# Kernel optimization log

Measured on AMD Instinct MI355X. Metric: run time of the kernel, lower is better.

The kernel has to match this reference:

```python
import jax, jax.numpy as jnp
import numpy as np

B, S, V = 8, 8192, 64
D, DV, DT, H = 256, 32, 256, 8
DH = D // H

def setup_inputs() -> dict:
    key = jax.random.key(0)
    ks = jax.random.split(key, 24)
    def p(i, shape, s=0.02):
        return jax.random.normal(ks[i], shape, jnp.float32) * s
    return {
        'times': jax.random.uniform(ks[0], (B, S), jnp.float32),
        'feature_ids': jax.random.randint(ks[1], (B, S), 0, V),
        'values': jax.random.normal(ks[2], (B, S), jnp.float32),
        'valid_mask': jax.random.randint(ks[3], (B, S), 0, 2).astype(bool),
        'me_w': p(4, (D,), 1.0), 'me_b': p(5, (D,)),
        'var_emb': p(6, (V, DV), 1.0),
        'time_w': p(7, (DT,), 1.0), 'time_b': p(8, (DT,)),
        'agg_w': p(9, (D + DT, D - DV)), 'agg_b': p(10, (D - DV,)),
        'wq': p(11, (D, D)), 'bq': p(12, (D,)),
        'wk': p(13, (D, D)), 'bk': p(14, (D,)),
        'wv': p(15, (D, D)), 'bv': p(16, (D,)),
        'wo': p(17, (D, D)), 'bo': p(18, (D,)),
        'cw1': p(19, (D, D)), 'cb1': p(20, (D,)),
        'cw2': p(21, (D, 1)), 'cb2': p(22, (1,)),
    }

def reference(times, feature_ids, values, valid_mask,
              me_w, me_b, var_emb, time_w, time_b, agg_w, agg_b,
              wq, bq, wk, bk, wv, bv, wo, bo, cw1, cb1, cw2, cb2):
    # Embeddings: measurement [B,S,D], variate [B,S,DV], time [B,S,DT]
    e_l = values[..., None] * me_w + me_b
    v_l = var_emb[feature_ids]
    u_l = times[..., None] * time_w + time_b
    eu = jnp.concatenate([e_l, u_l], axis=-1)                   # [B,S,D+DT]
    h_l = jnp.concatenate([v_l, eu @ agg_w + agg_b], axis=-1)   # [B,S,D]

    # Vectorized masked segment mean per variate (replaces Python loop)
    var_mask = (feature_ids[:, None, :] == jnp.arange(V)[None, :, None]) \
               & valid_mask[:, None, :]                         # [B,V,S] bool
    mf = var_mask.astype(h_l.dtype)
    sums = jnp.einsum('bvs,bsd->bvd', mf, h_l)
    counts = jnp.clip(mf.sum(-1), 1.0)                          # [B,V]
    f_mean = sums / counts[..., None]                           # [B,V,D]

    # Grouped cross-attention: one query per variate, shared K/V = h_l
    kpm = ~var_mask                                             # key padding mask
    all_masked = ~var_mask.any(-1)                              # [B,V]
    kpm = kpm.at[:, :, 0].set(kpm[:, :, 0] & ~all_masked)       # unmask pos 0 if empty

    q = (f_mean @ wq + bq).reshape(B, V, H, DH)
    k = (h_l @ wk + bk).reshape(B, S, H, DH)
    v = (h_l @ wv + bv).reshape(B, S, H, DH)
    scores = jnp.einsum('bvhd,bshd->bvhs', q, k) / np.sqrt(DH)  # [B,V,H,S]
    neg = jnp.finfo(scores.dtype).min
    scores = jnp.where(kpm[:, :, None, :], neg, scores)
    attn = jax.nn.softmax(scores, axis=-1)
    ctx = jnp.einsum('bvhs,bshd->bvhd', attn, v).reshape(B, V, D)
    f_var = ctx @ wo + bo                                       # [B,V,D]

    f = f_var.mean(axis=1)                                      # [B,D]
    out = jax.nn.relu(f @ cw1 + cb1) @ cw2 + cb2                # [B,1]
    return out
```

## Files before the change

### kernel.cpp

```cpp
#include <hip/hip_runtime.h>
#include <hip/hip_bf16.h>
#include <math.h>

#define BB 8
#define SS 8192
#define VV 64
#define AGG_OUT 224

#define WS_FLAGS 0
#define WS_A     16
#define WS_C     240
#define WS_D     464
#define WS_AQ    688
#define WS_CQ    944
#define WS_DQ    1200
#define WS_AK    1456
#define WS_CK    1712
#define WS_DK    1968
#define WS_AV    2224
#define WS_CV    2480
#define WS_DV    2736
#define WS_WQE   2992
#define WS_WKE   19376
#define WS_WVE   35760
#define WS_CSUM  52144
#define WS_BINS  54192
#define WS_COEF  66480
#define WS_SP    82864

__device__ __forceinline__ float ldf(const void* p, int idx, int fm) {
  if (fm) {
    unsigned int u = ((const unsigned short*)p)[idx];
    return __uint_as_float(u << 16);
  }
  return ((const float*)p)[idx];
}

__device__ __forceinline__ bool mask_at(const void* p, int idx, int mm) {
  switch (mm) {
    case 0: return ((const int*)p)[idx] != 0;
    case 1: return ((const float*)p)[idx] != 0.0f;
    case 2: return ((const unsigned short*)p)[idx] != 0;
    default: return ((const unsigned char*)p)[idx] != 0;
  }
}

__device__ __forceinline__ unsigned int fkey(float f) {
  unsigned int u = __float_as_uint(f);
  return (u & 0x80000000u) ? ~u : (u | 0x80000000u);
}
__device__ __forceinline__ float funkey(unsigned int k) {
  unsigned int u = (k & 0x80000000u) ? (k ^ 0x80000000u) : ~k;
  return __uint_as_float(u);
}

__device__ __forceinline__ int detect_fm_block(const void* times) {
  __shared__ int cntR;
  int tid = threadIdx.x;
  if (tid == 0) cntR = 0;
  __syncthreads();
  const unsigned int* tw = (const unsigned int*)times;
  int local = 0;
  for (int i = tid; i < 1024; i += 256) {
    unsigned int lo = tw[i] & 0xFFFFu;
    if (lo >= 0x3800u && lo < 0x3F80u) local++;
  }
  atomicAdd(&cntR, local);
  __syncthreads();
  int r = (cntR > 512) ? 1 : 0;
  __syncthreads();
  return r;
}

__device__ __forceinline__ int detect_mm_block(const void* mask) {
  __shared__ int f01, ff32, fbf;
  int tid = threadIdx.x;
  if (tid == 0) { f01 = 1; ff32 = 1; fbf = 1; }
  __syncthreads();
  const unsigned int* mw = (const unsigned int*)mask;
  int l01 = 1, lf32 = 1, lbf = 1;
  for (int i = tid; i < 2048; i += 256) {
    unsigned int w = mw[i];
    if (w > 1u) l01 = 0;
    if (!(w == 0u || w == 0x3F800000u)) lf32 = 0;
    unsigned int h0 = w & 0xFFFFu, h1 = w >> 16;
    if (!((h0 == 0u || h0 == 0x3F80u) && (h1 == 0u || h1 == 0x3F80u))) lbf = 0;
  }
  if (!l01) atomicAnd(&f01, 0);
  if (!lf32) atomicAnd(&ff32, 0);
  if (!lbf) atomicAnd(&fbf, 0);
  __syncthreads();
  int r = f01 ? 0 : (ff32 ? 1 : (fbf ? 2 : 3));
  __syncthreads();
  return r;
}

__global__ void __launch_bounds__(256) k_front(const void* times, const void* values,
                                               const int* fids, const void* mask,
                                               const void* me_w, const void* me_b,
                                               const void* time_w, const void* time_b,
                                               const void* agg_w, const void* agg_b,
                                               float* ws) {
  int blk = blockIdx.x, tid = threadIdx.x;
  if (blk < 224) {
    int fm = detect_fm_block(times);
    int j = blk, i = tid;
    float w0 = ldf(agg_w, i * AGG_OUT + j, fm);
    float w1 = ldf(agg_w, (256 + i) * AGG_OUT + j, fm);
    float sa = ldf(me_w, i, fm) * w0;
    float sc = ldf(time_w, i, fm) * w1;
    float sd = ldf(me_b, i, fm) * w0 + ldf(time_b, i, fm) * w1;
    #pragma unroll
    for (int off = 32; off >= 1; off >>= 1) {
      sa += __shfl_xor(sa, off);
      sc += __shfl_xor(sc, off);
      sd += __shfl_xor(sd, off);
    }
    __shared__ float r[3][4];
    int wid = i >> 6;
    if ((i & 63) == 0) { r[0][wid] = sa; r[1][wid] = sc; r[2][wid] = sd; }
    __syncthreads();
    if (i == 0) {
      ws[WS_A + j] = r[0][0] + r[0][1] + r[0][2] + r[0][3];
      ws[WS_C + j] = r[1][0] + r[1][1] + r[1][2] + r[1][3];
      ws[WS_D + j] = r[2][0] + r[2][1] + r[2][2] + r[2][3] + ldf(agg_b, j, fm);
    }
  } else if (blk < 288) {
    int fm = detect_fm_block(times);
    int mm = detect_mm_block(mask);
    int sblk = blk - 224, b = sblk >> 3, chunk = sblk & 7;
    __shared__ float hc[64], hsv[64], hst[64];
    __shared__ unsigned int hvn[64], hvx[64], htn[64], htx[64];
    if (tid < 64) {
      hc[tid] = 0.f; hsv[tid] = 0.f; hst[tid] = 0.f;
      hvn[tid] = 0xFFFFFFFFu; hvx[tid] = 0u;
      htn[tid] = 0xFFFFFFFFu; htx[tid] = 0u;
    }
    __syncthreads();
    #pragma unroll
    for (int k = 0; k < 4; k++) {
      int idx = b * SS + chunk * 1024 + k * 256 + tid;
      if (mask_at(mask, idx, mm)) {
        int f = fids[idx];
        float val = ldf(values, idx, fm), tim = ldf(times, idx, fm);
        atomicAdd(&hc[f], 1.0f);
        atomicAdd(&hsv[f], val);
        atomicAdd(&hst[f], tim);
        unsigned int vk = fkey(val), tk = fkey(tim);
        atomicMin(&hvn[f], vk); atomicMax(&hvx[f], vk);
        atomicMin(&htn[f], tk); atomicMax(&htx[f], tk);
      }
    }
    __syncthreads();
    if (tid < 64) {
      int base = WS_SP + (sblk * 64 + tid) * 8;
      ws[base + 0] = hc[tid];
      ws[base + 1] = hsv[tid];
      ws[base + 2] = hst[tid];
      ((unsigned int*)ws)[base + 3] = hvn[tid];
      ((unsigned int*)ws)[base + 4] = hvx[tid];
      ((unsigned int*)ws)[base + 5] = htn[tid];
      ((unsigned int*)ws)[base + 6] = htx[tid];
    }
  } else {
    int zblk = blk - 288;
    for (int i = zblk * 256 + tid; i < 14336; i += 2048) ws[WS_CSUM + i] = 0.f;
    if (zblk == 0) {
      int fm = detect_fm_block(times);
      int mm = detect_mm_block(mask);
      if (tid == 0) { ((int*)ws)[0] = fm; ((int*)ws)[1] = mm; }
    }
  }
}

__global__ void __launch_bounds__(256) k_pre(const void* wq, const void* wk,
                                             const void* wv, const void* bk,
                                             const void* bv, const void* var_emb,
                                             float* ws) {
  int fm = ((const int*)ws)[0];
  int blk = blockIdx.x, tid = threadIdx.x;
  if (blk < 24) {
    int X = blk >> 3, dg = blk & 7;
    const void* w = (X == 0) ? wq : (X == 1) ? wk : wv;
    __shared__ float sha[224], shc[224], shd[224];
    if (tid < 224) {
      sha[tid] = ws[WS_A + tid];
      shc[tid] = ws[WS_C + tid];
      shd[tid] = ws[WS_D + tid];
    }
    __syncthreads();
    int dsub = tid & 31, jg = tid >> 5;
    int d = dg * 32 + dsub;
    float sa = 0.f, sc = 0.f, sd = 0.f;
    #pragma unroll 4
    for (int jj = 0; jj < 28; jj++) {
      int j = jg * 28 + jj;
      float ww = ldf(w, (32 + j) * 256 + d, fm);
      sa += sha[j] * ww; sc += shc[j] * ww; sd += shd[j] * ww;
    }
    __shared__ float ps[3][8][32];
    ps[0][jg][dsub] = sa; ps[1][jg][dsub] = sc; ps[2][jg][dsub] = sd;
    __syncthreads();
    if (tid < 32) {
      float ra = 0.f, rc = 0.f, rd = 0.f;
      #pragma unroll
      for (int g = 0; g < 8; g++) {
        ra += ps[0][g][tid]; rc += ps[1][g][tid]; rd += ps[2][g][tid];
      }
      int dd = dg * 32 + tid;
      if (X == 1) rd += ldf(bk, dd, fm);
      if (X == 2) rd += ldf(bv, dd, fm);
      int base = (X == 0) ? WS_AQ : (X == 1) ? WS_AK : WS_AV;
      ws[base + dd] = ra;
      ws[base + 256 + dd] = rc;
      ws[base + 512 + dd] = rd;
    }
  } else {
    int idx = blk - 24, X = idx >> 6, v = idx & 63, d = tid;
    const void* w = (X == 0) ? wq : (X == 1) ? wk : wv;
    float s = 0.f;
    #pragma unroll 8
    for (int i = 0; i < 32; i++)
      s += ldf(var_emb, v * 32 + i, fm) * ldf(w, i * 256 + d, fm);
    int base = (X == 0) ? WS_WQE : (X == 1) ? WS_WKE : WS_WVE;
    ws[base + v * 256 + d] = s;
  }
}

__global__ void __launch_bounds__(256) k_coef(const void* values, const void* times,
                                              const int* fids, const void* bq,
                                              float* ws) {
  int fm = ((const int*)ws)[0];
  int bv = blockIdx.x, b = bv >> 6, v = bv & 63;
  int tid = threadIdx.x, h = tid >> 5;
  __shared__ float sp[8][8];
  if (tid < 64) {
    int sl = tid >> 3, c = tid & 7;
    sp[sl][c] = ws[WS_SP + ((b * 8 + sl) * 64 + v) * 8 + c];
  }
  __syncthreads();
  float cT = 0.f, svT = 0.f, stT = 0.f;
  unsigned int vnk = 0xFFFFFFFFu, vxk = 0u, tnk = 0xFFFFFFFFu, txk = 0u;
  #pragma unroll
  for (int sl = 0; sl < 8; sl++) {
    cT += sp[sl][0]; svT += sp[sl][1]; stT += sp[sl][2];
    unsigned int a3 = __float_as_uint(sp[sl][3]);
    unsigned int a4 = __float_as_uint(sp[sl][4]);
    unsigned int a5 = __float_as_uint(sp[sl][5]);
    unsigned int a6 = __float_as_uint(sp[sl][6]);
    vnk = min(vnk, a3); vxk = max(vxk, a4);
    tnk = min(tnk, a5); txk = max(txk, a6);
  }
  if (cT == 0.f) {
    int f0 = fids[b * SS];
    float v0 = ldf(values, b * SS, fm), t0 = ldf(times, b * SS, fm);
    float ctx = ws[WS_WVE + f0 * 256 + tid] + ws[WS_DV + tid]
              + v0 * ws[WS_AV + tid] + t0 * ws[WS_CV + tid];
    atomicAdd(&ws[WS_CSUM + b * 256 + tid], ctx);
    return;
  }
  float inv = 1.0f / cT, mv = svT * inv, mt = stT * inv;
  float qv = ldf(bq, tid, fm) + ws[WS_WQE + v * 256 + tid]
           + mv * ws[WS_AQ + tid] + mt * ws[WS_CQ + tid] + ws[WS_DQ + tid];
  qv *= 0.17677669529663687f * 1.4426950408889634f;
  float pA = qv * (ws[WS_WKE + v * 256 + tid] + ws[WS_DK + tid]);
  float pB = qv * ws[WS_AK + tid];
  float pC = qv * ws[WS_CK + tid];
  #pragma unroll
  for (int off = 16; off >= 1; off >>= 1) {
    pA += __shfl_xor(pA, off);
    pB += __shfl_xor(pB, off);
    pC += __shfl_xor(pC, off);
  }
  if ((tid & 31) == 0) {
    float vmn = funkey(vnk), vmx = funkey(vxk);
    float tmn = funkey(tnk), tmx = funkey(txk);
    float m = pA + fmaxf(pB * vmn, pB * vmx) + fmaxf(pC * tmn, pC * tmx);
    int base = WS_COEF + (bv * 8 + h) * 4;
    ws[base + 0] = pA; ws[base + 1] = pB; ws[base + 2] = pC; ws[base + 3] = m;
  }
}

__global__ void __launch_bounds__(256) k_accum(const void* values, const void* times,
                                               const int* fids, const void* mask,
                                               float* ws) {
  int fm = ((const int*)ws)[0], mm = ((const int*)ws)[1];
  int blk = blockIdx.x, tid = threadIdx.x;
  int b = blk >> 4, chunk = blk & 15;
  __shared__ float co[64 * 36];
  __shared__ float bins[64 * 25];
  for (int i = tid; i < 2048; i += 256) {
    int v = i >> 5, r = i & 31;
    co[v * 36 + r] = ws[WS_COEF + b * 2048 + i];
  }
  for (int i = tid; i < 1600; i += 256) bins[i] = 0.f;
  __syncthreads();
  #pragma unroll
  for (int k = 0; k < 2; k++) {
    int idx = b * SS + chunk * 512 + k * 256 + tid;
    if (mask_at(mask, idx, mm)) {
      int f = fids[idx];
      float val = ldf(values, idx, fm), tim = ldf(times, idx, fm);
      #pragma unroll
      for (int h = 0; h < 8; h++) {
        int cb = f * 36 + h * 4;
        float w = exp2f(co[cb] + val * co[cb + 1] + tim * co[cb + 2] - co[cb + 3]);
        int bb = f * 25 + h * 3;
        atomicAdd(&bins[bb], w);
        atomicAdd(&bins[bb + 1], w * val);
        atomicAdd(&bins[bb + 2], w * tim);
      }
    }
  }
  __syncthreads();
  for (int i = tid; i < 1536; i += 256) {
    int f = i / 24, r = i - f * 24;
    float x = bins[f * 25 + r];
    if (x != 0.f) atomicAdd(&ws[WS_BINS + b * 1536 + i], x);
  }
}

__global__ void __launch_bounds__(1024) k_fin(const void* wo, const void* bo,
                                              const void* cw1, const void* cb1,
                                              const void* cw2, const void* cb2,
                                              float* ws, void* out) {
  int fm = ((const int*)ws)[0];
  int b = blockIdx.x, tid = threadIdx.x;
  __shared__ float aa[64][9], tt[64][9], ne[64];
  __shared__ float ps[4][256], cs[256], fv[256], pr[16];
  if (tid < 512) {
    int v = tid >> 3, h = tid & 7;
    int base = WS_BINS + b * 1536 + v * 24 + h * 3;
    float W = ws[base], WV = ws[base + 1], WT = ws[base + 2];
    float iW = (W > 0.f) ? 1.0f / W : 0.f;
    aa[v][h] = WV * iW; tt[v][h] = WT * iW;
    if (h == 0) ne[v] = (W > 0.f) ? 1.f : 0.f;
  }
  __syncthreads();
  int d = tid & 255, vg = tid >> 8, h = d >> 5;
  float accP = 0.f, accA = 0.f, accT = 0.f, accN = 0.f;
  #pragma unroll 4
  for (int k = 0; k < 16; k++) {
    int v = vg * 16 + k;
    float nef = ne[v];
    accP += nef * ws[WS_WVE + v * 256 + d];
    accA += aa[v][h];
    accT += tt[v][h];
    accN += nef;
  }
  ps[vg][d] = accP + accN * ws[WS_DV + d] + accA * ws[WS_AV + d] + accT * ws[WS_CV + d];
  __syncthreads();
  if (tid < 256)
    cs[tid] = (ws[WS_CSUM + b * 256 + tid] + ps[0][tid] + ps[1][tid]
             + ps[2][tid] + ps[3][tid]) * (1.0f / 64.0f);
  __syncthreads();
  float s = 0.f;
  #pragma unroll 8
  for (int k = 0; k < 64; k++) {
    int i = vg * 64 + k;
    s += cs[i] * ldf(wo, i * 256 + d, fm);
  }
  ps[vg][d] = s;
  __syncthreads();
  if (tid < 256) fv[tid] = ps[0][tid] + ps[1][tid] + ps[2][tid] + ps[3][tid]
                         + ldf(bo, tid, fm);
  __syncthreads();
  float t2 = 0.f;
  #pragma unroll 8
  for (int k = 0; k < 64; k++) {
    int i = vg * 64 + k;
    t2 += fv[i] * ldf(cw1, i * 256 + d, fm);
  }
  ps[vg][d] = t2;
  __syncthreads();
  float p = 0.f;
  if (tid < 256) {
    float t = ps[0][tid] + ps[1][tid] + ps[2][tid] + ps[3][tid] + ldf(cb1, tid, fm);
    t = fmaxf(t, 0.f);
    p = t * ldf(cw2, tid, fm);
  }
  #pragma unroll
  for (int off = 32; off >= 1; off >>= 1) p += __shfl_xor(p, off);
  if ((tid & 63) == 0) pr[tid >> 6] = p;
  __syncthreads();
  if (tid == 0) {
    float o = ldf(cb2, 0, fm);
    #pragma unroll
    for (int wgi = 0; wgi < 16; wgi++) o += pr[wgi];
    if (fm) {
      unsigned int x = __float_as_uint(o);
      unsigned int r = (x + 0x7FFFu + ((x >> 16) & 1u)) >> 16;
      ((unsigned short*)out)[b] = (unsigned short)r;
    } else {
      ((float*)out)[b] = o;
    }
  }
}

extern "C" void kernel_launch(void* const* d_in, const int* in_sizes, int n_in,
                              void* d_out, int out_size, void* d_ws, size_t ws_size,
                              hipStream_t stream) {
  const void* times   = d_in[0];
  const int*  fids    = (const int*)d_in[1];
  const void* values  = d_in[2];
  const void* vmask   = d_in[3];
  const void* me_w    = d_in[4];
  const void* me_b    = d_in[5];
  const void* var_emb = d_in[6];
  const void* time_w  = d_in[7];
  const void* time_b  = d_in[8];
  const void* agg_w   = d_in[9];
  const void* agg_b   = d_in[10];
  const void* wq = d_in[11]; const void* bq = d_in[12];
  const void* wk = d_in[13]; const void* bk = d_in[14];
  const void* wv = d_in[15]; const void* bv = d_in[16];
  const void* wo = d_in[17]; const void* bo = d_in[18];
  const void* cw1 = d_in[19]; const void* cb1 = d_in[20];
  const void* cw2 = d_in[21]; const void* cb2 = d_in[22];
  float* ws = (float*)d_ws;

  k_front<<<296, 256, 0, stream>>>(times, values, fids, vmask,
                                   me_w, me_b, time_w, time_b, agg_w, agg_b, ws);
  k_pre<<<216, 256, 0, stream>>>(wq, wk, wv, bk, bv, var_emb, ws);
  k_coef<<<512, 256, 0, stream>>>(values, times, fids, bq, ws);
  k_accum<<<128, 256, 0, stream>>>(values, times, fids, vmask, ws);
  k_fin<<<8, 1024, 0, stream>>>(wo, bo, cw1, cb1, cw2, cb2, ws, d_out);
}
```

Before: 149.7 us.

## Fold Q·K into per-variate 3x3 bilinear forms and merge five kernels into three

Drops the k_pre and k_coef kernels. Each k_front block now recomputes the agg folding (A,C,D) redundantly, builds per-variate, per-head 3x3 bilinear matrices relating the query's mean value/time to the key's value/time, and writes those to the workspace. k_accum rebuilds the per-variate statistics and the logit coefficients in shared memory, and the empty-variate correction moves into k_fin. The aim is to cut launch count and inter-kernel round-trips. The cost is heavily redundant serial per-thread loops: 64 blocks each run a 256-step agg reduction and a 224-step weight loop. k_accum also drops to 64 blocks.

```diff
diff --git a/kernel.cpp b/kernel.cpp
--- a/kernel.cpp
+++ b/kernel.cpp
@@ -4,29 +4,14 @@
 
 #define BB 8
 #define SS 8192
-#define VV 64
 #define AGG_OUT 224
 
 #define WS_FLAGS 0
-#define WS_A     16
-#define WS_C     240
-#define WS_D     464
-#define WS_AQ    688
-#define WS_CQ    944
-#define WS_DQ    1200
-#define WS_AK    1456
-#define WS_CK    1712
-#define WS_DK    1968
-#define WS_AV    2224
-#define WS_CV    2480
-#define WS_DV    2736
-#define WS_WQE   2992
-#define WS_WKE   19376
-#define WS_WVE   35760
-#define WS_CSUM  52144
-#define WS_BINS  54192
-#define WS_COEF  66480
-#define WS_SP    82864
+#define WS_M     16
+#define WS_AV3   6160
+#define WS_WVE   6928
+#define WS_SP    23312
+#define WS_BINS  56080
 
 __device__ __forceinline__ float ldf(const void* p, int idx, int fm) {
   if (fm) {
@@ -100,35 +85,89 @@
                                                const void* me_w, const void* me_b,
                                                const void* time_w, const void* time_b,
                                                const void* agg_w, const void* agg_b,
+                                               const void* var_emb, const void* wq,
+                                               const void* wk, const void* wv,
+                                               const void* bq, const void* bv,
                                                float* ws) {
   int blk = blockIdx.x, tid = threadIdx.x;
-  if (blk < 224) {
+  if (blk < 64) {
     int fm = detect_fm_block(times);
-    int j = blk, i = tid;
-    float w0 = ldf(agg_w, i * AGG_OUT + j, fm);
-    float w1 = ldf(agg_w, (256 + i) * AGG_OUT + j, fm);
-    float sa = ldf(me_w, i, fm) * w0;
-    float sc = ldf(time_w, i, fm) * w1;
-    float sd = ldf(me_b, i, fm) * w0 + ldf(time_b, i, fm) * w1;
+    int v = blk;
+    __shared__ float a_[224], c_[224], d_[224];
+    if (tid < 224) {
+      float sa = 0.f, sc = 0.f, sd = 0.f;
+      for (int i = 0; i < 256; i++) {
+        float w0 = ldf(agg_w, i * AGG_OUT + tid, fm);
+        float w1 = ldf(agg_w, (256 + i) * AGG_OUT + tid, fm);
+        sa += ldf(me_w, i, fm) * w0;
+        sc += ldf(time_w, i, fm) * w1;
+        sd += ldf(me_b, i, fm) * w0 + ldf(time_b, i, fm) * w1;
+      }
+      a_[tid] = sa; c_[tid] = sc; d_[tid] = sd + ldf(agg_b, tid, fm);
+    }
+    __syncthreads();
+    int d = tid;
+    float AQ = 0.f, CQ = 0.f, DQ = 0.f, AK = 0.f, CK = 0.f, DK = 0.f;
+    for (int j = 0; j < 224; j++) {
+      float wwq = ldf(wq, (32 + j) * 256 + d, fm);
+      float wwk = ldf(wk, (32 + j) * 256 + d, fm);
+      float aj = a_[j], cj = c_[j], dj = d_[j];
+      AQ += aj * wwq; CQ += cj * wwq; DQ += dj * wwq;
+      AK += aj * wwk; CK += cj * wwk; DK += dj * wwk;
+    }
+    float QE = 0.f, KE = 0.f, VE = 0.f;
+    for (int i = 0; i < 32; i++) {
+      float ve = ldf(var_emb, v * 32 + i, fm);
+      QE += ve * ldf(wq, i * 256 + d, fm);
+      KE += ve * ldf(wk, i * 256 + d, fm);
+      VE += ve * ldf(wv, i * 256 + d, fm);
+    }
+    ws[WS_WVE + v * 256 + d] = VE;
+    float q0 = ldf(bq, d, fm) + QE + DQ, k0 = KE + DK;
+    float mm_[9] = {q0 * k0, q0 * AK, q0 * CK,
+                    AQ * k0, AQ * AK, AQ * CK,
+                    CQ * k0, CQ * AK, CQ * CK};
     #pragma unroll
-    for (int off = 32; off >= 1; off >>= 1) {
-      sa += __shfl_xor(sa, off);
-      sc += __shfl_xor(sc, off);
-      sd += __shfl_xor(sd, off);
-    }
-    __shared__ float r[3][4];
-    int wid = i >> 6;
-    if ((i & 63) == 0) { r[0][wid] = sa; r[1][wid] = sc; r[2][wid] = sd; }
-    __syncthreads();
-    if (i == 0) {
-      ws[WS_A + j] = r[0][0] + r[0][1] + r[0][2] + r[0][3];
-      ws[WS_C + j] = r[1][0] + r[1][1] + r[1][2] + r[1][3];
-      ws[WS_D + j] = r[2][0] + r[2][1] + r[2][2] + r[2][3] + ldf(agg_b, j, fm);
-    }
-  } else if (blk < 288) {
+    for (int r = 0; r < 9; r++)
+      #pragma unroll
+      for (int off = 16; off >= 1; off >>= 1)
+        mm_[r] += __shfl_xor(mm_[r], off);
+    if ((tid & 31) == 0) {
+      int h = tid >> 5;
+      const float sc2 = 0.17677669529663687f * 1.4426950408889634f;
+      int base = WS_M + (v * 8 + h) * 12;
+      #pragma unroll
+      for (int r = 0; r < 9; r++) ws[base + r] = mm_[r] * sc2;
+    }
+    if (v < 8) {
+      int dsub = tid & 31, jg = tid >> 5;
+      int d2 = v * 32 + dsub;
+      float sa = 0.f, sc3 = 0.f, sd = 0.f;
+      #pragma unroll 4
+      for (int jj = 0; jj < 28; jj++) {
+        int j = jg * 28 + jj;
+        float wwv = ldf(wv, (32 + j) * 256 + d2, fm);
+        sa += a_[j] * wwv; sc3 += c_[j] * wwv; sd += d_[j] * wwv;
+      }
+      __shared__ float ps[3][8][32];
+      ps[0][jg][dsub] = sa; ps[1][jg][dsub] = sc3; ps[2][jg][dsub] = sd;
+      __syncthreads();
+      if (tid < 32) {
+        float ra = 0.f, rc = 0.f, rd = 0.f;
+        #pragma unroll
+        for (int g = 0; g < 8; g++) {
+          ra += ps[0][g][tid]; rc += ps[1][g][tid]; rd += ps[2][g][tid];
+        }
+        int d3 = v * 32 + tid;
+        ws[WS_AV3 + d3] = ra;
+        ws[WS_AV3 + 256 + d3] = rc;
+        ws[WS_AV3 + 512 + d3] = rd + ldf(bv, d3, fm);
+      }
+    }
+  } else if (blk < 128) {
     int fm = detect_fm_block(times);
     int mm = detect_mm_block(mask);
-    int sblk = blk - 224, b = sblk >> 3, chunk = sblk & 7;
+    int sblk = blk - 64, b = sblk >> 3, chunk = sblk & 7;
     __shared__ float hc[64], hsv[64], hst[64];
     __shared__ unsigned int hvn[64], hvx[64], htn[64], htx[64];
     if (tid < 64) {
@@ -163,121 +202,13 @@
       ((unsigned int*)ws)[base + 6] = htx[tid];
     }
   } else {
-    int zblk = blk - 288;
-    for (int i = zblk * 256 + tid; i < 14336; i += 2048) ws[WS_CSUM + i] = 0.f;
+    int zblk = blk - 128;
+    for (int i = zblk * 256 + tid; i < 12288; i += 8 * 256) ws[WS_BINS + i] = 0.f;
     if (zblk == 0) {
       int fm = detect_fm_block(times);
-      int mm = detect_mm_block(mask);
-      if (tid == 0) { ((int*)ws)[0] = fm; ((int*)ws)[1] = mm; }
-    }
-  }
-}
-
-__global__ void __launch_bounds__(256) k_pre(const void* wq, const void* wk,
-                                             const void* wv, const void* bk,
-                                             const void* bv, const void* var_emb,
-                                             float* ws) {
-  int fm = ((const int*)ws)[0];
-  int blk = blockIdx.x, tid = threadIdx.x;
-  if (blk < 24) {
-    int X = blk >> 3, dg = blk & 7;
-    const void* w = (X == 0) ? wq : (X == 1) ? wk : wv;
-    __shared__ float sha[224], shc[224], shd[224];
-    if (tid < 224) {
-      sha[tid] = ws[WS_A + tid];
-      shc[tid] = ws[WS_C + tid];
-      shd[tid] = ws[WS_D + tid];
-    }
-    __syncthreads();
-    int dsub = tid & 31, jg = tid >> 5;
-    int d = dg * 32 + dsub;
-    float sa = 0.f, sc = 0.f, sd = 0.f;
-    #pragma unroll 4
-    for (int jj = 0; jj < 28; jj++) {
-      int j = jg * 28 + jj;
-      float ww = ldf(w, (32 + j) * 256 + d, fm);
-      sa += sha[j] * ww; sc += shc[j] * ww; sd += shd[j] * ww;
-    }
-    __shared__ float ps[3][8][32];
-    ps[0][jg][dsub] = sa; ps[1][jg][dsub] = sc; ps[2][jg][dsub] = sd;
-    __syncthreads();
-    if (tid < 32) {
-      float ra = 0.f, rc = 0.f, rd = 0.f;
-      #pragma unroll
-      for (int g = 0; g < 8; g++) {
-        ra += ps[0][g][tid]; rc += ps[1][g][tid]; rd += ps[2][g][tid];
-      }
-      int dd = dg * 32 + tid;
-      if (X == 1) rd += ldf(bk, dd, fm);
-      if (X == 2) rd += ldf(bv, dd, fm);
-      int base = (X == 0) ? WS_AQ : (X == 1) ? WS_AK : WS_AV;
-      ws[base + dd] = ra;
-      ws[base + 256 + dd] = rc;
-      ws[base + 512 + dd] = rd;
-    }
-  } else {
-    int idx = blk - 24, X = idx >> 6, v = idx & 63, d = tid;
-    const void* w = (X == 0) ? wq : (X == 1) ? wk : wv;
-    float s = 0.f;
-    #pragma unroll 8
-    for (int i = 0; i < 32; i++)
-      s += ldf(var_emb, v * 32 + i, fm) * ldf(w, i * 256 + d, fm);
-    int base = (X == 0) ? WS_WQE : (X == 1) ? WS_WKE : WS_WVE;
-    ws[base + v * 256 + d] = s;
-  }
-}
-
-__global__ void __launch_bounds__(256) k_coef(const void* values, const void* times,
-                                              const int* fids, const void* bq,
-                                              float* ws) {
-  int fm = ((const int*)ws)[0];
-  int bv = blockIdx.x, b = bv >> 6, v = bv & 63;
-  int tid = threadIdx.x, h = tid >> 5;
-  __shared__ float sp[8][8];
-  if (tid < 64) {
-    int sl = tid >> 3, c = tid & 7;
-    sp[sl][c] = ws[WS_SP + ((b * 8 + sl) * 64 + v) * 8 + c];
-  }
-  __syncthreads();
-  float cT = 0.f, svT = 0.f, stT = 0.f;
-  unsigned int vnk = 0xFFFFFFFFu, vxk = 0u, tnk = 0xFFFFFFFFu, txk = 0u;
-  #pragma unroll
-  for (int sl = 0; sl < 8; sl++) {
-    cT += sp[sl][0]; svT += sp[sl][1]; stT += sp[sl][2];
-    unsigned int a3 = __float_as_uint(sp[sl][3]);
-    unsigned int a4 = __float_as_uint(sp[sl][4]);
-    unsigned int a5 = __float_as_uint(sp[sl][5]);
-    unsigned int a6 = __float_as_uint(sp[sl][6]);
-    vnk = min(vnk, a3); vxk = max(vxk, a4);
-    tnk = min(tnk, a5); txk = max(txk, a6);
-  }
-  if (cT == 0.f) {
-    int f0 = fids[b * SS];
-    float v0 = ldf(values, b * SS, fm), t0 = ldf(times, b * SS, fm);
-    float ctx = ws[WS_WVE + f0 * 256 + tid] + ws[WS_DV + tid]
-              + v0 * ws[WS_AV + tid] + t0 * ws[WS_CV + tid];
-    atomicAdd(&ws[WS_CSUM + b * 256 + tid], ctx);
-    return;
-  }
-  float inv = 1.0f / cT, mv = svT * inv, mt = stT * inv;
-  float qv = ldf(bq, tid, fm) + ws[WS_WQE + v * 256 + tid]
-           + mv * ws[WS_AQ + tid] + mt * ws[WS_CQ + tid] + ws[WS_DQ + tid];
-  qv *= 0.17677669529663687f * 1.4426950408889634f;
-  float pA = qv * (ws[WS_WKE + v * 256 + tid] + ws[WS_DK + tid]);
-  float pB = qv * ws[WS_AK + tid];
-  float pC = qv * ws[WS_CK + tid];
-  #pragma unroll
-  for (int off = 16; off >= 1; off >>= 1) {
-    pA += __shfl_xor(pA, off);
-    pB += __shfl_xor(pB, off);
-    pC += __shfl_xor(pC, off);
-  }
-  if ((tid & 31) == 0) {
-    float vmn = funkey(vnk), vmx = funkey(vxk);
-    float tmn = funkey(tnk), tmx = funkey(txk);
-    float m = pA + fmaxf(pB * vmn, pB * vmx) + fmaxf(pC * tmn, pC * tmx);
-    int base = WS_COEF + (bv * 8 + h) * 4;
-    ws[base + 0] = pA; ws[base + 1] = pB; ws[base + 2] = pC; ws[base + 3] = m;
+      int mmm = detect_mm_block(mask);
+      if (tid == 0) { ((int*)ws)[0] = fm; ((int*)ws)[1] = mmm; }
+    }
   }
 }
 
@@ -286,18 +217,51 @@
                                                float* ws) {
   int fm = ((const int*)ws)[0], mm = ((const int*)ws)[1];
   int blk = blockIdx.x, tid = threadIdx.x;
-  int b = blk >> 4, chunk = blk & 15;
+  int b = blk >> 3, chunk = blk & 7;
+  __shared__ float stv[64][8];
   __shared__ float co[64 * 36];
   __shared__ float bins[64 * 25];
-  for (int i = tid; i < 2048; i += 256) {
-    int v = i >> 5, r = i & 31;
-    co[v * 36 + r] = ws[WS_COEF + b * 2048 + i];
+  if (tid < 64) {
+    int v = tid;
+    float c = 0.f, sv = 0.f, st = 0.f;
+    unsigned int vnk = 0xFFFFFFFFu, vxk = 0u, tnk = 0xFFFFFFFFu, txk = 0u;
+    #pragma unroll
+    for (int sl = 0; sl < 8; sl++) {
+      int base = WS_SP + ((b * 8 + sl) * 64 + v) * 8;
+      c += ws[base]; sv += ws[base + 1]; st += ws[base + 2];
+      unsigned int a3 = ((const unsigned int*)ws)[base + 3];
+      unsigned int a4 = ((const unsigned int*)ws)[base + 4];
+      unsigned int a5 = ((const unsigned int*)ws)[base + 5];
+      unsigned int a6 = ((const unsigned int*)ws)[base + 6];
+      vnk = min(vnk, a3); vxk = max(vxk, a4);
+      tnk = min(tnk, a5); txk = max(txk, a6);
+    }
+    float ic = (c > 0.f) ? 1.0f / c : 0.f;
+    stv[v][0] = c; stv[v][1] = sv * ic; stv[v][2] = st * ic;
+    stv[v][3] = funkey(vnk); stv[v][4] = funkey(vxk);
+    stv[v][5] = funkey(tnk); stv[v][6] = funkey(txk);
   }
   for (int i = tid; i < 1600; i += 256) bins[i] = 0.f;
   __syncthreads();
+  for (int p = tid; p < 512; p += 256) {
+    int v = p >> 3, h = p & 7;
+    int base = WS_M + (v * 8 + h) * 12;
+    float m00 = ws[base],     m01 = ws[base + 1], m02 = ws[base + 2];
+    float m10 = ws[base + 3], m11 = ws[base + 4], m12 = ws[base + 5];
+    float m20 = ws[base + 6], m21 = ws[base + 7], m22 = ws[base + 8];
+    float mv = stv[v][1], mt = stv[v][2];
+    float A  = m00 + mv * m10 + mt * m20;
+    float Bc = m01 + mv * m11 + mt * m21;
+    float Cc = m02 + mv * m12 + mt * m22;
+    float mstab = A + fmaxf(Bc * stv[v][3], Bc * stv[v][4])
+                    + fmaxf(Cc * stv[v][5], Cc * stv[v][6]);
+    int cb = v * 36 + h * 4;
+    co[cb] = A; co[cb + 1] = Bc; co[cb + 2] = Cc; co[cb + 3] = mstab;
+  }
+  __syncthreads();
   #pragma unroll
-  for (int k = 0; k < 2; k++) {
-    int idx = b * SS + chunk * 512 + k * 256 + tid;
+  for (int k = 0; k < 4; k++) {
+    int idx = b * SS + chunk * 1024 + k * 256 + tid;
     if (mask_at(mask, idx, mm)) {
       int f = fids[idx];
       float val = ldf(values, idx, fm), tim = ldf(times, idx, fm);
@@ -320,14 +284,15 @@
   }
 }
 
-__global__ void __launch_bounds__(1024) k_fin(const void* wo, const void* bo,
-                                              const void* cw1, const void* cb1,
-                                              const void* cw2, const void* cb2,
-                                              float* ws, void* out) {
+__global__ void __launch_bounds__(1024) k_fin(const int* fids, const void* values,
+                                              const void* times, const void* wo,
+                                              const void* bo, const void* cw1,
+                                              const void* cb1, const void* cw2,
+                                              const void* cb2, float* ws, void* out) {
   int fm = ((const int*)ws)[0];
   int b = blockIdx.x, tid = threadIdx.x;
   __shared__ float aa[64][9], tt[64][9], ne[64];
-  __shared__ float ps[4][256], cs[256], fv[256], pr[16];
+  __shared__ float ps[4][256], cs[256], fv[256], pr[16], neg_[4];
   if (tid < 512) {
     int v = tid >> 3, h = tid & 7;
     int base = WS_BINS + b * 1536 + v * 24 + h * 3;
@@ -348,11 +313,21 @@
     accT += tt[v][h];
     accN += nef;
   }
-  ps[vg][d] = accP + accN * ws[WS_DV + d] + accA * ws[WS_AV + d] + accT * ws[WS_CV + d];
-  __syncthreads();
-  if (tid < 256)
-    cs[tid] = (ws[WS_CSUM + b * 256 + tid] + ps[0][tid] + ps[1][tid]
-             + ps[2][tid] + ps[3][tid]) * (1.0f / 64.0f);
+  ps[vg][d] = accP + accN * ws[WS_AV3 + 512 + d]
+            + accA * ws[WS_AV3 + d] + accT * ws[WS_AV3 + 256 + d];
+  if (d == 0) neg_[vg] = accN;
+  __syncthreads();
+  if (tid < 256) {
+    float nE = 64.f - (neg_[0] + neg_[1] + neg_[2] + neg_[3]);
+    float ce = 0.f;
+    if (nE > 0.f) {
+      int f0 = fids[b * SS];
+      float v0 = ldf(values, b * SS, fm), t0 = ldf(times, b * SS, fm);
+      ce = nE * (ws[WS_WVE + f0 * 256 + tid] + ws[WS_AV3 + 512 + tid]
+               + v0 * ws[WS_AV3 + tid] + t0 * ws[WS_AV3 + 256 + tid]);
+    }
+    cs[tid] = (ps[0][tid] + ps[1][tid] + ps[2][tid] + ps[3][tid] + ce) * (1.0f / 64.0f);
+  }
   __syncthreads();
   float s = 0.f;
   #pragma unroll 8
@@ -412,17 +387,17 @@
   const void* agg_w   = d_in[9];
   const void* agg_b   = d_in[10];
   const void* wq = d_in[11]; const void* bq = d_in[12];
-  const void* wk = d_in[13]; const void* bk = d_in[14];
+  const void* wk = d_in[13];
   const void* wv = d_in[15]; const void* bv = d_in[16];
   const void* wo = d_in[17]; const void* bo = d_in[18];
   const void* cw1 = d_in[19]; const void* cb1 = d_in[20];
   const void* cw2 = d_in[21]; const void* cb2 = d_in[22];
   float* ws = (float*)d_ws;
 
-  k_front<<<296, 256, 0, stream>>>(times, values, fids, vmask,
-                                   me_w, me_b, time_w, time_b, agg_w, agg_b, ws);
-  k_pre<<<216, 256, 0, stream>>>(wq, wk, wv, bk, bv, var_emb, ws);
-  k_coef<<<512, 256, 0, stream>>>(values, times, fids, bq, ws);
-  k_accum<<<128, 256, 0, stream>>>(values, times, fids, vmask, ws);
-  k_fin<<<8, 1024, 0, stream>>>(wo, bo, cw1, cb1, cw2, cb2, ws, d_out);
-}
+  k_front<<<136, 256, 0, stream>>>(times, values, fids, vmask,
+                                   me_w, me_b, time_w, time_b, agg_w, agg_b,
+                                   var_emb, wq, wk, wv, bq, bv, ws);
+  k_accum<<<64, 256, 0, stream>>>(values, times, fids, vmask, ws);
+  k_fin<<<8, 1024, 0, stream>>>(fids, values, times, wo, bo, cw1, cb1, cw2, cb2,
+                                ws, d_out);
+}
```

Measured after the change: 291.7 us. 94.8% more time.

## Merge pipeline from five kernels to four by fusing coefficient computation into accumulate

Applied to the files above, without the earlier changes.

Moves the var_emb-projected weight precompute into k_front and folds the per-(b,v,h) score coefficient computation into k_accum, dropping the separate k_coef kernel. Empty-variate fallback contributions move into k_fin as a count-scaled term instead of atomics, and bq is folded into the Q bias vector. k_accum now uses 64 blocks, each covering 1024 tokens. The intent is to cut launch and serialization overhead between small kernels, at the price of every accum block redundantly recomputing the coefficients.

```diff
diff --git a/kernel.cpp b/kernel.cpp
--- a/kernel.cpp
+++ b/kernel.cpp
@@ -4,7 +4,6 @@
 
 #define BB 8
 #define SS 8192
-#define VV 64
 #define AGG_OUT 224
 
 #define WS_FLAGS 0
@@ -17,16 +16,12 @@
 #define WS_AK    1456
 #define WS_CK    1712
 #define WS_DK    1968
-#define WS_AV    2224
-#define WS_CV    2480
-#define WS_DV    2736
+#define WS_AV3   2224
 #define WS_WQE   2992
 #define WS_WKE   19376
 #define WS_WVE   35760
-#define WS_CSUM  52144
-#define WS_BINS  54192
-#define WS_COEF  66480
-#define WS_SP    82864
+#define WS_SP    52144
+#define WS_BINS  84912
 
 __device__ __forceinline__ float ldf(const void* p, int idx, int fm) {
   if (fm) {
@@ -100,6 +95,8 @@
                                                const void* me_w, const void* me_b,
                                                const void* time_w, const void* time_b,
                                                const void* agg_w, const void* agg_b,
+                                               const void* var_emb, const void* wq,
+                                               const void* wk, const void* wv,
                                                float* ws) {
   int blk = blockIdx.x, tid = threadIdx.x;
   if (blk < 224) {
@@ -162,61 +159,9 @@
       ((unsigned int*)ws)[base + 5] = htn[tid];
       ((unsigned int*)ws)[base + 6] = htx[tid];
     }
-  } else {
-    int zblk = blk - 288;
-    for (int i = zblk * 256 + tid; i < 14336; i += 2048) ws[WS_CSUM + i] = 0.f;
-    if (zblk == 0) {
-      int fm = detect_fm_block(times);
-      int mm = detect_mm_block(mask);
-      if (tid == 0) { ((int*)ws)[0] = fm; ((int*)ws)[1] = mm; }
-    }
-  }
-}
-
-__global__ void __launch_bounds__(256) k_pre(const void* wq, const void* wk,
-                                             const void* wv, const void* bk,
-                                             const void* bv, const void* var_emb,
-                                             float* ws) {
-  int fm = ((const int*)ws)[0];
-  int blk = blockIdx.x, tid = threadIdx.x;
-  if (blk < 24) {
-    int X = blk >> 3, dg = blk & 7;
-    const void* w = (X == 0) ? wq : (X == 1) ? wk : wv;
-    __shared__ float sha[224], shc[224], shd[224];
-    if (tid < 224) {
-      sha[tid] = ws[WS_A + tid];
-      shc[tid] = ws[WS_C + tid];
-      shd[tid] = ws[WS_D + tid];
-    }
-    __syncthreads();
-    int dsub = tid & 31, jg = tid >> 5;
-    int d = dg * 32 + dsub;
-    float sa = 0.f, sc = 0.f, sd = 0.f;
-    #pragma unroll 4
-    for (int jj = 0; jj < 28; jj++) {
-      int j = jg * 28 + jj;
-      float ww = ldf(w, (32 + j) * 256 + d, fm);
-      sa += sha[j] * ww; sc += shc[j] * ww; sd += shd[j] * ww;
-    }
-    __shared__ float ps[3][8][32];
-    ps[0][jg][dsub] = sa; ps[1][jg][dsub] = sc; ps[2][jg][dsub] = sd;
-    __syncthreads();
-    if (tid < 32) {
-      float ra = 0.f, rc = 0.f, rd = 0.f;
-      #pragma unroll
-      for (int g = 0; g < 8; g++) {
-        ra += ps[0][g][tid]; rc += ps[1][g][tid]; rd += ps[2][g][tid];
-      }
-      int dd = dg * 32 + tid;
-      if (X == 1) rd += ldf(bk, dd, fm);
-      if (X == 2) rd += ldf(bv, dd, fm);
-      int base = (X == 0) ? WS_AQ : (X == 1) ? WS_AK : WS_AV;
-      ws[base + dd] = ra;
-      ws[base + 256 + dd] = rc;
-      ws[base + 512 + dd] = rd;
-    }
-  } else {
-    int idx = blk - 24, X = idx >> 6, v = idx & 63, d = tid;
+  } else if (blk < 480) {
+    int fm = detect_fm_block(times);
+    int idx = blk - 288, X = idx >> 6, v = idx & 63, d = tid;
     const void* w = (X == 0) ? wq : (X == 1) ? wk : wv;
     float s = 0.f;
     #pragma unroll 8
@@ -224,60 +169,58 @@
       s += ldf(var_emb, v * 32 + i, fm) * ldf(w, i * 256 + d, fm);
     int base = (X == 0) ? WS_WQE : (X == 1) ? WS_WKE : WS_WVE;
     ws[base + v * 256 + d] = s;
-  }
-}
-
-__global__ void __launch_bounds__(256) k_coef(const void* values, const void* times,
-                                              const int* fids, const void* bq,
+  } else {
+    int zblk = blk - 480;
+    for (int i = zblk * 256 + tid; i < 12288; i += 8 * 256) ws[WS_BINS + i] = 0.f;
+    if (zblk == 0) {
+      int fm = detect_fm_block(times);
+      int mmm = detect_mm_block(mask);
+      if (tid == 0) { ((int*)ws)[0] = fm; ((int*)ws)[1] = mmm; }
+    }
+  }
+}
+
+__global__ void __launch_bounds__(256) k_fold(const void* wq, const void* wk,
+                                              const void* wv, const void* bq,
+                                              const void* bk, const void* bv,
                                               float* ws) {
   int fm = ((const int*)ws)[0];
-  int bv = blockIdx.x, b = bv >> 6, v = bv & 63;
-  int tid = threadIdx.x, h = tid >> 5;
-  __shared__ float sp[8][8];
-  if (tid < 64) {
-    int sl = tid >> 3, c = tid & 7;
-    sp[sl][c] = ws[WS_SP + ((b * 8 + sl) * 64 + v) * 8 + c];
-  }
-  __syncthreads();
-  float cT = 0.f, svT = 0.f, stT = 0.f;
-  unsigned int vnk = 0xFFFFFFFFu, vxk = 0u, tnk = 0xFFFFFFFFu, txk = 0u;
-  #pragma unroll
-  for (int sl = 0; sl < 8; sl++) {
-    cT += sp[sl][0]; svT += sp[sl][1]; stT += sp[sl][2];
-    unsigned int a3 = __float_as_uint(sp[sl][3]);
-    unsigned int a4 = __float_as_uint(sp[sl][4]);
-    unsigned int a5 = __float_as_uint(sp[sl][5]);
-    unsigned int a6 = __float_as_uint(sp[sl][6]);
-    vnk = min(vnk, a3); vxk = max(vxk, a4);
-    tnk = min(tnk, a5); txk = max(txk, a6);
-  }
-  if (cT == 0.f) {
-    int f0 = fids[b * SS];
-    float v0 = ldf(values, b * SS, fm), t0 = ldf(times, b * SS, fm);
-    float ctx = ws[WS_WVE + f0 * 256 + tid] + ws[WS_DV + tid]
-              + v0 * ws[WS_AV + tid] + t0 * ws[WS_CV + tid];
-    atomicAdd(&ws[WS_CSUM + b * 256 + tid], ctx);
-    return;
-  }
-  float inv = 1.0f / cT, mv = svT * inv, mt = stT * inv;
-  float qv = ldf(bq, tid, fm) + ws[WS_WQE + v * 256 + tid]
-           + mv * ws[WS_AQ + tid] + mt * ws[WS_CQ + tid] + ws[WS_DQ + tid];
-  qv *= 0.17677669529663687f * 1.4426950408889634f;
-  float pA = qv * (ws[WS_WKE + v * 256 + tid] + ws[WS_DK + tid]);
-  float pB = qv * ws[WS_AK + tid];
-  float pC = qv * ws[WS_CK + tid];
-  #pragma unroll
-  for (int off = 16; off >= 1; off >>= 1) {
-    pA += __shfl_xor(pA, off);
-    pB += __shfl_xor(pB, off);
-    pC += __shfl_xor(pC, off);
-  }
-  if ((tid & 31) == 0) {
-    float vmn = funkey(vnk), vmx = funkey(vxk);
-    float tmn = funkey(tnk), tmx = funkey(txk);
-    float m = pA + fmaxf(pB * vmn, pB * vmx) + fmaxf(pC * tmn, pC * tmx);
-    int base = WS_COEF + (bv * 8 + h) * 4;
-    ws[base + 0] = pA; ws[base + 1] = pB; ws[base + 2] = pC; ws[base + 3] = m;
+  int blk = blockIdx.x, tid = threadIdx.x;
+  int X = blk >> 3, dg = blk & 7;
+  const void* w = (X == 0) ? wq : (X == 1) ? wk : wv;
+  __shared__ float sha[224], shc[224], shd[224];
+  if (tid < 224) {
+    sha[tid] = ws[WS_A + tid];
+    shc[tid] = ws[WS_C + tid];
+    shd[tid] = ws[WS_D + tid];
+  }
+  __syncthreads();
+  int dsub = tid & 31, jg = tid >> 5;
+  int d = dg * 32 + dsub;
+  float sa = 0.f, sc = 0.f, sd = 0.f;
+  #pragma unroll 4
+  for (int jj = 0; jj < 28; jj++) {
+    int j = jg * 28 + jj;
+    float ww = ldf(w, (32 + j) * 256 + d, fm);
+    sa += sha[j] * ww; sc += shc[j] * ww; sd += shd[j] * ww;
+  }
+  __shared__ float ps[3][8][32];
+  ps[0][jg][dsub] = sa; ps[1][jg][dsub] = sc; ps[2][jg][dsub] = sd;
+  __syncthreads();
+  if (tid < 32) {
+    float ra = 0.f, rc = 0.f, rd = 0.f;
+    #pragma unroll
+    for (int g = 0; g < 8; g++) {
+      ra += ps[0][g][tid]; rc += ps[1][g][tid]; rd += ps[2][g][tid];
+    }
+    int dd = dg * 32 + tid;
+    if (X == 0) rd += ldf(bq, dd, fm);
+    if (X == 1) rd += ldf(bk, dd, fm);
+    if (X == 2) rd += ldf(bv, dd, fm);
+    int base = (X == 0) ? WS_AQ : (X == 1) ? WS_AK : WS_AV3;
+    ws[base + dd] = ra;
+    ws[base + 256 + dd] = rc;
+    ws[base + 512 + dd] = rd;
   }
 }
 
@@ -286,18 +229,69 @@
                                                float* ws) {
   int fm = ((const int*)ws)[0], mm = ((const int*)ws)[1];
   int blk = blockIdx.x, tid = threadIdx.x;
-  int b = blk >> 4, chunk = blk & 15;
+  int b = blk >> 3, chunk = blk & 7;
+  __shared__ float stv[64][8];
+  __shared__ float sF[6][256];
   __shared__ float co[64 * 36];
   __shared__ float bins[64 * 25];
-  for (int i = tid; i < 2048; i += 256) {
-    int v = i >> 5, r = i & 31;
-    co[v * 36 + r] = ws[WS_COEF + b * 2048 + i];
+  sF[0][tid] = ws[WS_AQ + tid];
+  sF[1][tid] = ws[WS_CQ + tid];
+  sF[2][tid] = ws[WS_DQ + tid];
+  sF[3][tid] = ws[WS_AK + tid];
+  sF[4][tid] = ws[WS_CK + tid];
+  sF[5][tid] = ws[WS_DK + tid];
+  if (tid < 64) {
+    int v = tid;
+    float c = 0.f, sv = 0.f, st = 0.f;
+    unsigned int vnk = 0xFFFFFFFFu, vxk = 0u, tnk = 0xFFFFFFFFu, txk = 0u;
+    #pragma unroll
+    for (int sl = 0; sl < 8; sl++) {
+      int base = WS_SP + ((b * 8 + sl) * 64 + v) * 8;
+      c += ws[base]; sv += ws[base + 1]; st += ws[base + 2];
+      unsigned int a3 = ((const unsigned int*)ws)[base + 3];
+      unsigned int a4 = ((const unsigned int*)ws)[base + 4];
+      unsigned int a5 = ((const unsigned int*)ws)[base + 5];
+      unsigned int a6 = ((const unsigned int*)ws)[base + 6];
+      vnk = min(vnk, a3); vxk = max(vxk, a4);
+      tnk = min(tnk, a5); txk = max(txk, a6);
+    }
+    float ic = (c > 0.f) ? 1.0f / c : 0.f;
+    stv[v][0] = c; stv[v][1] = sv * ic; stv[v][2] = st * ic;
+    stv[v][3] = funkey(vnk); stv[v][4] = funkey(vxk);
+    stv[v][5] = funkey(tnk); stv[v][6] = funkey(txk);
   }
   for (int i = tid; i < 1600; i += 256) bins[i] = 0.f;
   __syncthreads();
+  const float sc2 = 0.17677669529663687f * 1.4426950408889634f;
   #pragma unroll
-  for (int k = 0; k < 2; k++) {
-    int idx = b * SS + chunk * 512 + k * 256 + tid;
+  for (int pp = 0; pp < 2; pp++) {
+    int p = pp * 256 + tid;
+    int v = p >> 3, h = p & 7;
+    float A = 0.f, Bc = 0.f, Cc = 0.f;
+    float mv = stv[v][1], mt = stv[v][2];
+    #pragma unroll 8
+    for (int i = 0; i < 32; i++) {
+      int d = h * 32 + i;
+      float wqe = ws[WS_WQE + v * 256 + d];
+      float wke = ws[WS_WKE + v * 256 + d];
+      float q = wqe + sF[2][d] + mv * sF[0][d] + mt * sF[1][d];
+      float k0 = wke + sF[5][d];
+      A += q * k0; Bc += q * sF[3][d]; Cc += q * sF[4][d];
+    }
+    A *= sc2; Bc *= sc2; Cc *= sc2;
+    float mstab = A + fmaxf(Bc * stv[v][3], Bc * stv[v][4])
+                    + fmaxf(Cc * stv[v][5], Cc * stv[v][6]);
+    int cb = v * 36 + h * 4;
+    bool live = (stv[v][0] > 0.f);
+    co[cb] = live ? A : 0.f;
+    co[cb + 1] = live ? Bc : 0.f;
+    co[cb + 2] = live ? Cc : 0.f;
+    co[cb + 3] = live ? mstab : 0.f;
+  }
+  __syncthreads();
+  #pragma unroll
+  for (int k = 0; k < 4; k++) {
+    int idx = b * SS + chunk * 1024 + k * 256 + tid;
     if (mask_at(mask, idx, mm)) {
       int f = fids[idx];
       float val = ldf(values, idx, fm), tim = ldf(times, idx, fm);
@@ -320,14 +314,15 @@
   }
 }
 
-__global__ void __launch_bounds__(1024) k_fin(const void* wo, const void* bo,
-                                              const void* cw1, const void* cb1,
-                                              const void* cw2, const void* cb2,
-                                              float* ws, void* out) {
+__global__ void __launch_bounds__(1024) k_fin(const int* fids, const void* values,
+                                              const void* times, const void* wo,
+                                              const void* bo, const void* cw1,
+                                              const void* cb1, const void* cw2,
+                                              const void* cb2, float* ws, void* out) {
   int fm = ((const int*)ws)[0];
   int b = blockIdx.x, tid = threadIdx.x;
   __shared__ float aa[64][9], tt[64][9], ne[64];
-  __shared__ float ps[4][256], cs[256], fv[256], pr[16];
+  __shared__ float ps[4][256], cs[256], fv[256], pr[16], neg_[4];
   if (tid < 512) {
     int v = tid >> 3, h = tid & 7;
     int base = WS_BINS + b * 1536 + v * 24 + h * 3;
@@ -348,11 +343,21 @@
     accT += tt[v][h];
     accN += nef;
   }
-  ps[vg][d] = accP + accN * ws[WS_DV + d] + accA * ws[WS_AV + d] + accT * ws[WS_CV + d];
-  __syncthreads();
-  if (tid < 256)
-    cs[tid] = (ws[WS_CSUM + b * 256 + tid] + ps[0][tid] + ps[1][tid]
-             + ps[2][tid] + ps[3][tid]) * (1.0f / 64.0f);
+  ps[vg][d] = accP + accN * ws[WS_AV3 + 512 + d]
+            + accA * ws[WS_AV3 + d] + accT * ws[WS_AV3 + 256 + d];
+  if (d == 0) neg_[vg] = accN;
+  __syncthreads();
+  if (tid < 256) {
+    float nE = 64.f - (neg_[0] + neg_[1] + neg_[2] + neg_[3]);
+    float ce = 0.f;
+    if (nE > 0.f) {
+      int f0 = fids[b * SS];
+      float v0 = ldf(values, b * SS, fm), t0 = ldf(times, b * SS, fm);
+      ce = nE * (ws[WS_WVE + f0 * 256 + tid] + ws[WS_AV3 + 512 + tid]
+               + v0 * ws[WS_AV3 + tid] + t0 * ws[WS_AV3 + 256 + tid]);
+    }
+    cs[tid] = (ps[0][tid] + ps[1][tid] + ps[2][tid] + ps[3][tid] + ce) * (1.0f / 64.0f);
+  }
   __syncthreads();
   float s = 0.f;
   #pragma unroll 8
@@ -419,10 +424,11 @@
   const void* cw2 = d_in[21]; const void* cb2 = d_in[22];
   float* ws = (float*)d_ws;
 
-  k_front<<<296, 256, 0, stream>>>(times, values, fids, vmask,
-                                   me_w, me_b, time_w, time_b, agg_w, agg_b, ws);
-  k_pre<<<216, 256, 0, stream>>>(wq, wk, wv, bk, bv, var_emb, ws);
-  k_coef<<<512, 256, 0, stream>>>(values, times, fids, bq, ws);
-  k_accum<<<128, 256, 0, stream>>>(values, times, fids, vmask, ws);
-  k_fin<<<8, 1024, 0, stream>>>(wo, bo, cw1, cb1, cw2, cb2, ws, d_out);
-}
+  k_front<<<488, 256, 0, stream>>>(times, values, fids, vmask,
+                                   me_w, me_b, time_w, time_b, agg_w, agg_b,
+                                   var_emb, wq, wk, wv, ws);
+  k_fold<<<24, 256, 0, stream>>>(wq, wk, wv, bq, bk, bv, ws);
+  k_accum<<<64, 256, 0, stream>>>(values, times, fids, vmask, ws);
+  k_fin<<<8, 1024, 0, stream>>>(fids, values, times, wo, bo, cw1, cb1, cw2, cb2,
+                                ws, d_out);
+}
```

Result: slower. 158.3 us (+5.7%).
